# Performance work log

Measured on AMD Instinct MI355X. Metric: run time of the kernel, lower is better.

The kernel has to match this reference:

```python
import jax, jax.numpy as jnp
import numpy as np

SINKHORN_ITERS = 8
TEMPERATURE = 1.0
EPS = 1e-6


def sinkhorn(t):
    # log-domain Sinkhorn normalization, matching torch: log(clamp(t, min=eps)) / temp
    t = jnp.log(jnp.clip(t, EPS)) / TEMPERATURE
    for _ in range(SINKHORN_ITERS):
        t = t - jax.nn.logsumexp(t, axis=-2, keepdims=True)  # over tokens n
        t = t - jax.nn.logsumexp(t, axis=-1, keepdims=True)  # over experts e
    return jnp.exp(t)


def setup_inputs() -> dict:
    key = jax.random.key(0)
    k1, k2, k3 = jax.random.split(key, 3)
    B, N, D, E = 4, 4096, 1024, 8
    x = jax.random.normal(k1, (B, N, D), dtype=jnp.float32)
    gate_w = jax.random.normal(k2, (D, E), dtype=jnp.float32) * (D ** -0.5)
    experts = jax.random.normal(k3, (E, D, D), dtype=jnp.float32) * (D ** -0.5)
    return {"x": x, "gate_w": gate_w, "experts": experts}


def reference(x, gate_w, experts):
    B, N, D = x.shape
    E = gate_w.shape[-1]
    M = N // E  # tokens per expert

    gate_logits = jnp.einsum('bnd,de->bne', x, gate_w)
    competitive_gates = sinkhorn(gate_logits)  # b n e

    # topk along token dim (-2): transpose to (b,e,n), top_k along last axis
    vals, idx = jax.lax.top_k(jnp.swapaxes(competitive_gates, -1, -2), M)  # b e m
    gate_values = jnp.swapaxes(vals, -1, -2)   # b m e
    routed_indices = jnp.swapaxes(idx, -1, -2)  # b m e (int32)

    b_idx = jnp.arange(B)[:, None, None]  # (b,1,1)
    routed = x[b_idx, routed_indices]     # b m e d
    routed = jnp.transpose(routed, (2, 0, 1, 3))  # e b m d

    outputs = jnp.einsum('ebmd,edf->ebmf', routed, experts)  # e b m d
    outputs = outputs * jnp.transpose(gate_values, (2, 0, 1))[..., None]  # * (e b m 1)

    vals_bmed = jnp.transpose(outputs, (1, 2, 0, 3))  # b m e d
    routed_back = jnp.zeros_like(x).at[b_idx, routed_indices].set(vals_bmed)
    return routed_back
```

## Files before the change

### kernel.cpp

```cpp
#include <hip/hip_runtime.h>
#include <hip/hip_bf16.h>
#include <stdint.h>

typedef short s16x8 __attribute__((ext_vector_type(8)));
typedef float f32x4 __attribute__((ext_vector_type(4)));
typedef unsigned short u16;
typedef unsigned int u32;
typedef unsigned long long u64;

__device__ __forceinline__ float bf2f(u16 v){
  union { u32 u; float f; } c; c.u = ((u32)v) << 16; return c.f;
}

__device__ __forceinline__ u16 f2bf(float f){
  u32 u = __float_as_uint(f);
  u32 r = (u + 0x7FFFu + ((u >> 16) & 1u)) >> 16;
  return (u16)r;
}

__device__ __forceinline__ uint4 pack8(float4 a, float4 b){
  union { uint4 v; u16 s[8]; } o;
  o.s[0]=f2bf(a.x); o.s[1]=f2bf(a.y); o.s[2]=f2bf(a.z); o.s[3]=f2bf(a.w);
  o.s[4]=f2bf(b.x); o.s[5]=f2bf(b.y); o.s[6]=f2bf(b.z); o.s[7]=f2bf(b.w);
  return o.v;
}

__device__ __forceinline__ void gll16(const u16* g, u16* l){
  __builtin_amdgcn_global_load_lds((const __attribute__((address_space(1))) u32*)g,
                                   (__attribute__((address_space(3))) u32*)l, 16, 0, 0);
}

__global__ __launch_bounds__(1024) void k_prep(const void* __restrict__ xv,
                                               const void* __restrict__ gwv,
                                               const void* __restrict__ Wv,
                                               u16* __restrict__ xb,
                                               u16* __restrict__ WT,
                                               float* __restrict__ gates,
                                               int* __restrict__ winner,
                                               int* __restrict__ flag,
                                               uint4* __restrict__ out,
                                               int out_size, int mode){
  __shared__ __align__(16) char smem[36864];
  __shared__ float wacc[16][8];
  __shared__ int   dred[16];
  int bx = blockIdx.x;
  int tid = threadIdx.x;
  int wave = tid >> 6, lane = tid & 63;

  int cnt = 0;
  {
    const u32* xw = (const u32*)xv;
    #pragma unroll
    for (int i = 0; i < 4; i++){
      u32 w = xw[(i << 10) + tid];
      cnt += (((w >> 7) & 0xFF) >= 140) ? 1 : 0;
    }
    #pragma unroll
    for (int off = 32; off; off >>= 1) cnt += __shfl_xor(cnt, off, 64);
    if (lane == 0) dred[wave] = cnt;
  }
  __syncthreads();
  int tot = 0;
  #pragma unroll
  for (int w2 = 0; w2 < 16; w2++) tot += dred[w2];
  int is_f32 = (tot > 256) ? 1 : 0;
  if (bx == 0 && tid == 0) *flag = is_f32;

  if (bx < 2048){
    if (bx < 16) winner[(bx << 10) + tid] = -1;
    float4* gw_swz = (float4*)smem;
    {
      int r = tid;
      float g0,g1,g2,g3,g4,g5,g6,g7;
      if (is_f32){
        const float* gw = (const float*)gwv + ((size_t)r << 3);
        float4 u = *(const float4*)gw;
        float4 v = *(const float4*)(gw + 4);
        g0=u.x; g1=u.y; g2=u.z; g3=u.w; g4=v.x; g5=v.y; g6=v.z; g7=v.w;
      } else {
        union { uint4 v; u16 s[8]; } wu;
        wu.v = *(const uint4*)((const u16*)gwv + ((size_t)r << 3));
        g0=bf2f(wu.s[0]); g1=bf2f(wu.s[1]); g2=bf2f(wu.s[2]); g3=bf2f(wu.s[3]);
        g4=bf2f(wu.s[4]); g5=bf2f(wu.s[5]); g6=bf2f(wu.s[6]); g7=bf2f(wu.s[7]);
      }
      int p = r >> 3, j = r & 7;
      gw_swz[(p << 4) + (((j << 1)    ) ^ (p & 15))] = make_float4(g0,g1,g2,g3);
      gw_swz[(p << 4) + (((j << 1) | 1) ^ (p & 15))] = make_float4(g4,g5,g6,g7);
    }

    int tl = tid >> 7, pos = tid & 127;
    size_t base = ((((size_t)bx << 3) + tl) << 10) + ((size_t)pos << 3);
    float xf[8];
    if (is_f32){
      const float* xr = (const float*)xv + base;
      float4 u = *(const float4*)xr;
      float4 v = *(const float4*)(xr + 4);
      xf[0]=u.x; xf[1]=u.y; xf[2]=u.z; xf[3]=u.w;
      xf[4]=v.x; xf[5]=v.y; xf[6]=v.z; xf[7]=v.w;
      if (mode) *(uint4*)(xb + base) = pack8(u, v);
    } else {
      uint4 raw = *(const uint4*)((const u16*)xv + base);
      union { uint4 v; u16 s[8]; } xu; xu.v = raw;
      #pragma unroll
      for (int k = 0; k < 8; k++) xf[k] = bf2f(xu.s[k]);
      if (mode) *(uint4*)(xb + base) = raw;
    }
    __syncthreads();

    float a0=0,a1=0,a2=0,a3=0,a4=0,a5=0,a6=0,a7=0;
    #pragma unroll
    for (int j = 0; j < 8; j++){
      float4 wA = gw_swz[(pos << 4) + (((j << 1)    ) ^ (pos & 15))];
      float4 wB = gw_swz[(pos << 4) + (((j << 1) | 1) ^ (pos & 15))];
      float xv8 = xf[j];
      a0 += xv8*wA.x; a1 += xv8*wA.y; a2 += xv8*wA.z; a3 += xv8*wA.w;
      a4 += xv8*wB.x; a5 += xv8*wB.y; a6 += xv8*wB.z; a7 += xv8*wB.w;
    }
    int s1 = lane & 1;
    float k0 = s1 ? a4 : a0, g0 = s1 ? a0 : a4;
    float k1 = s1 ? a5 : a1, g1 = s1 ? a1 : a5;
    float k2 = s1 ? a6 : a2, g2 = s1 ? a2 : a6;
    float k3 = s1 ? a7 : a3, g3 = s1 ? a3 : a7;
    k0 += __shfl_xor(g0, 1, 64); k1 += __shfl_xor(g1, 1, 64);
    k2 += __shfl_xor(g2, 1, 64); k3 += __shfl_xor(g3, 1, 64);
    int s2 = (lane >> 1) & 1;
    float m0 = s2 ? k2 : k0, h0 = s2 ? k0 : k2;
    float m1 = s2 ? k3 : k1, h1 = s2 ? k1 : k3;
    m0 += __shfl_xor(h0, 2, 64); m1 += __shfl_xor(h1, 2, 64);
    int s3 = (lane >> 2) & 1;
    float r = s3 ? m1 : m0, h = s3 ? m0 : m1;
    r += __shfl_xor(h, 4, 64);
    r += __shfl_xor(r, 8, 64);
    r += __shfl_xor(r, 16, 64);
    r += __shfl_xor(r, 32, 64);
    if (lane < 8){
      int e = ((lane & 1) << 2) | (lane & 2) | ((lane >> 2) & 1);
      wacc[wave][e] = r;
    }
    __syncthreads();
    if (tid < 64){
      int tt = tid >> 3, e = tid & 7;
      float v = wacc[(tt << 1)][e] + wacc[(tt << 1) | 1][e];
      gates[((((size_t)bx << 3) + tt) << 3) + e] = v;
    }
    return;
  }

  if (mode == 0){
    int rb = bx - 2048;
    size_t words = (size_t)out_size >> (is_f32 ? 0 : 1);
    size_t n4 = words >> 2;
    size_t i = (size_t)rb * 1024 + tid;
    uint4 z = make_uint4(0, 0, 0, 0);
    for (; i < n4; i += (size_t)512 * 1024) out[i] = z;
    return;
  }

  {
    int rb = bx - 2048;
    int sub = tid >> 8;
    int t = tid & 255;
    int g = (rb << 2) + sub;
    int e = g >> 8, t2 = g & 255;
    int td = (t2 >> 4) << 6, tf = (t2 & 15) << 6;
    u16 (*tile)[72] = (u16(*)[72])(smem + (size_t)sub * (64 * 72 * 2));
    #pragma unroll
    for (int i = 0; i < 2; i++){
      int id = t + (i << 8);
      int row = id >> 3, c8 = id & 7;
      size_t src = ((size_t)(e*1024 + td + row))*1024 + tf + (c8 << 3);
      uint4 v;
      if (is_f32){
        const float* wf = (const float*)Wv;
        v = pack8(*(const float4*)(wf + src), *(const float4*)(wf + src + 4));
      } else {
        v = *(const uint4*)((const u16*)Wv + src);
      }
      *(uint4*)&tile[row][c8 << 3] = v;
    }
    __syncthreads();
    #pragma unroll
    for (int i = 0; i < 2; i++){
      int id = t + (i << 8);
      int frow = id >> 3, c8 = id & 7;
      union { uint4 v; u16 s[8]; } o;
      #pragma unroll
      for (int j = 0; j < 8; j++) o.s[j] = tile[(c8 << 3) + j][frow];
      *(uint4*)(WT + ((size_t)(e*1024 + tf + frow))*1024 + td + (c8 << 3)) = o.v;
    }
  }
}

__global__ __launch_bounds__(1024) void k_sinkhorn(float* __restrict__ gates){
  __shared__ float wred[128];
  __shared__ float lbc[8];
  int bx = blockIdx.x;
  int tid = threadIdx.x;
  int wave = tid >> 6, lane = tid & 63;
  float* gb = gates + ((size_t)bx << 15);
  float4 va[4], vb[4];
  #pragma unroll
  for (int q = 0; q < 4; q++){
    float* gp = gb + (((q << 10) + tid) << 3);
    float4 a = *(const float4*)gp;
    float4 b = *(const float4*)(gp + 4);
    a.x=fmaxf(a.x,1e-6f); a.y=fmaxf(a.y,1e-6f); a.z=fmaxf(a.z,1e-6f); a.w=fmaxf(a.w,1e-6f);
    b.x=fmaxf(b.x,1e-6f); b.y=fmaxf(b.y,1e-6f); b.z=fmaxf(b.z,1e-6f); b.w=fmaxf(b.w,1e-6f);
    va[q]=a; vb[q]=b;
  }
  for (int it = 0; it < 8; it++){
    float s0 = ((va[0].x+va[1].x)+(va[2].x+va[3].x));
    float s1 = ((va[0].y+va[1].y)+(va[2].y+va[3].y));
    float s2 = ((va[0].z+va[1].z)+(va[2].z+va[3].z));
    float s3 = ((va[0].w+va[1].w)+(va[2].w+va[3].w));
    float s4 = ((vb[0].x+vb[1].x)+(vb[2].x+vb[3].x));
    float s5 = ((vb[0].y+vb[1].y)+(vb[2].y+vb[3].y));
    float s6 = ((vb[0].z+vb[1].z)+(vb[2].z+vb[3].z));
    float s7 = ((vb[0].w+vb[1].w)+(vb[2].w+vb[3].w));
    #pragma unroll
    for (int off = 32; off; off >>= 1){
      s0 += __shfl_xor(s0, off, 64); s1 += __shfl_xor(s1, off, 64);
      s2 += __shfl_xor(s2, off, 64); s3 += __shfl_xor(s3, off, 64);
      s4 += __shfl_xor(s4, off, 64); s5 += __shfl_xor(s5, off, 64);
      s6 += __shfl_xor(s6, off, 64); s7 += __shfl_xor(s7, off, 64);
    }
    if (lane == 0){
      wred[(wave<<3)+0]=s0; wred[(wave<<3)+1]=s1; wred[(wave<<3)+2]=s2; wred[(wave<<3)+3]=s3;
      wred[(wave<<3)+4]=s4; wred[(wave<<3)+5]=s5; wred[(wave<<3)+6]=s6; wred[(wave<<3)+7]=s7;
    }
    __syncthreads();
    if (tid < 8){
      float S = 0.f;
      #pragma unroll
      for (int w2 = 0; w2 < 16; w2++) S += wred[(w2 << 3) + tid];
      lbc[tid] = 1.0f / S;
    }
    __syncthreads();
    float i0=lbc[0], i1=lbc[1], i2=lbc[2], i3=lbc[3];
    float i4=lbc[4], i5=lbc[5], i6=lbc[6], i7=lbc[7];
    #pragma unroll
    for (int q = 0; q < 4; q++){
      float4 a = va[q], b = vb[q];
      a.x*=i0; a.y*=i1; a.z*=i2; a.w*=i3;
      b.x*=i4; b.y*=i5; b.z*=i6; b.w*=i7;
      float rs = ((a.x+a.y)+(a.z+a.w)) + ((b.x+b.y)+(b.z+b.w));
      float ir = 1.0f / rs;
      a.x*=ir; a.y*=ir; a.z*=ir; a.w*=ir;
      b.x*=ir; b.y*=ir; b.z*=ir; b.w*=ir;
      va[q]=a; vb[q]=b;
    }
  }
  #pragma unroll
  for (int q = 0; q < 4; q++){
    float* gp = gb + (((q << 10) + tid) << 3);
    *(float4*)gp = va[q];
    *(float4*)(gp + 4) = vb[q];
  }
}

__global__ __launch_bounds__(256) void k_rank(const float* __restrict__ gates,
                                              int* __restrict__ routed, int* __restrict__ winner){
  __shared__ u32 ord_s[4096];
  __shared__ u32 cnt_s[1024];
  int bx = blockIdx.x;
  int be = bx >> 5;
  int b = be >> 3, e = be & 7;
  int slice = bx & 31;
  int tid = threadIdx.x;
  const float* gb = gates + (size_t)b * (4096 * 8);
  for (int i = tid; i < 4096; i += 256){
    float v = gb[(i << 3) + e];
    u32 fb = __float_as_uint(v);
    ord_s[i] = fb ^ ((fb >> 31) ? 0xFFFFFFFFu : 0x80000000u);
  }
  __syncthreads();

  int tg = tid & 31;
  int js = tid >> 5;
  int i0 = (slice << 7) + (tg << 2);
  int gchunk = i0 & ~7;
  u32 v0 = ord_s[i0], v1 = ord_s[i0+1], v2 = ord_s[i0+2], v3 = ord_s[i0+3];
  int jlo = js << 9, jhi = jlo + 512;
  int c0 = 0, c1 = 0, c2 = 0, c3 = 0;

  int endA = min(jhi, gchunk);
  for (int j = jlo; j < endA; j += 8){
    uint4 w0 = *(const uint4*)&ord_s[j];
    uint4 w1 = *(const uint4*)&ord_s[j + 4];
    c0 += (w0.x>=v0)+(w0.y>=v0)+(w0.z>=v0)+(w0.w>=v0)+(w1.x>=v0)+(w1.y>=v0)+(w1.z>=v0)+(w1.w>=v0);
    c1 += (w0.x>=v1)+(w0.y>=v1)+(w0.z>=v1)+(w0.w>=v1)+(w1.x>=v1)+(w1.y>=v1)+(w1.z>=v1)+(w1.w>=v1);
    c2 += (w0.x>=v2)+(w0.y>=v2)+(w0.z>=v2)+(w0.w>=v2)+(w1.x>=v2)+(w1.y>=v2)+(w1.z>=v2)+(w1.w>=v2);
    c3 += (w0.x>=v3)+(w0.y>=v3)+(w0.z>=v3)+(w0.w>=v3)+(w1.x>=v3)+(w1.y>=v3)+(w1.z>=v3)+(w1.w>=v3);
  }
  int begB = max(jlo, gchunk + 8);
  for (int j = begB; j < jhi; j += 8){
    uint4 w0 = *(const uint4*)&ord_s[j];
    uint4 w1 = *(const uint4*)&ord_s[j + 4];
    c0 += (w0.x>v0)+(w0.y>v0)+(w0.z>v0)+(w0.w>v0)+(w1.x>v0)+(w1.y>v0)+(w1.z>v0)+(w1.w>v0);
    c1 += (w0.x>v1)+(w0.y>v1)+(w0.z>v1)+(w0.w>v1)+(w1.x>v1)+(w1.y>v1)+(w1.z>v1)+(w1.w>v1);
    c2 += (w0.x>v2)+(w0.y>v2)+(w0.z>v2)+(w0.w>v2)+(w1.x>v2)+(w1.y>v2)+(w1.z>v2)+(w1.w>v2);
    c3 += (w0.x>v3)+(w0.y>v3)+(w0.z>v3)+(w0.w>v3)+(w1.x>v3)+(w1.y>v3)+(w1.z>v3)+(w1.w>v3);
  }
  if (gchunk >= jlo && gchunk < jhi){
    int base_off = i0 & 7;
    #pragma unroll
    for (int jj = 0; jj < 8; jj++){
      u32 w = ord_s[gchunk + jj];
      c0 += (jj < base_off + 0) ? (w >= v0) : (w > v0);
      c1 += (jj < base_off + 1) ? (w >= v1) : (w > v1);
      c2 += (jj < base_off + 2) ? (w >= v2) : (w > v2);
      c3 += (jj < base_off + 3) ? (w >= v3) : (w > v3);
    }
  }
  int lt = tg << 2;
  cnt_s[(js << 7) + lt + 0] = c0;
  cnt_s[(js << 7) + lt + 1] = c1;
  cnt_s[(js << 7) + lt + 2] = c2;
  cnt_s[(js << 7) + lt + 3] = c3;
  __syncthreads();
  if (tid < 128){
    int rank = 0;
    #pragma unroll
    for (int s = 0; s < 8; s++) rank += cnt_s[(s << 7) + tid];
    int i = (slice << 7) + tid;
    if (rank < 512){
      routed[(be << 9) + rank] = i;
      atomicMax(&winner[(b << 12) + i], (rank << 3) | e);
    }
  }
}

__global__ __launch_bounds__(256) void k_gemm_fast(const u16* __restrict__ xb, const u16* __restrict__ WT,
                                                   const float* __restrict__ gates,
                                                   const int* __restrict__ routed,
                                                   const int* __restrict__ winner,
                                                   const int* __restrict__ flag,
                                                   void* __restrict__ outv){
  __shared__ u16 As[128 * 32];
  __shared__ u16 Bs[128 * 32];
  __shared__ int   tok_s[128];
  __shared__ float gate_s[128];
  __shared__ int   flg_s[128];
  int is_f32 = *flag;
  int bx = blockIdx.x;
  int tid = threadIdx.x;

  if (bx >= 1024){
    int zb = bx - 1024;
    #pragma unroll 1
    for (int i = 0; i < 128; i++){
      int g = (zb << 7) + i;
      if (winner[g] < 0){
        size_t rbase = ((size_t)g) << 10;
        if (is_f32){
          float* o = (float*)outv;
          *(float4*)(o + rbase + (tid << 2)) = make_float4(0.f, 0.f, 0.f, 0.f);
        } else {
          u16* o = (u16*)outv;
          uint2 z; z.x = 0; z.y = 0;
          *(uint2*)(o + rbase + (tid << 2)) = z;
        }
      }
    }
    return;
  }

  int e = bx & 7;
  int rest = bx >> 3;
  int b = rest >> 5;
  int tile = rest & 31;
  int mt = tile & 3, nt = tile >> 2;
  int w = tid >> 6, lane = tid & 63;
  int quad = lane >> 4, l16 = lane & 15;

  const int* idx_base = routed + (((b << 3) + e) << 9) + (mt << 7);

  if (tid < 128){
    int tok = idx_base[tid];
    int mg  = (mt << 7) + tid;
    int win = winner[(b << 12) + tok];
    tok_s[tid]  = tok;
    flg_s[tid]  = (win == ((mg << 3) | e)) ? 1 : 0;
    gate_s[tid] = gates[((((size_t)b << 12) + tok) << 3) + e];
  }
  __syncthreads();

  int r0 = tid >> 2;
  int ch = tid & 3;
  int r1 = r0 + 64;
  int swz = ch ^ ((r0 >> 1) & 3);
  const u16* gA0 = xb + ((((size_t)b << 12) + tok_s[r0]) << 10) + (swz << 3);
  const u16* gA1 = xb + ((((size_t)b << 12) + tok_s[r1]) << 10) + (swz << 3);
  int f0 = nt << 7;
  const u16* gB0 = WT + ((((size_t)e << 10) + f0 + r0) << 10) + (swz << 3);
  const u16* gB1 = WT + ((((size_t)e << 10) + f0 + r1) << 10) + (swz << 3);
  u16* lA0 = As + (w << 9);
  u16* lA1 = As + 2048 + (w << 9);
  u16* lB0 = Bs + (w << 9);
  u16* lB1 = Bs + 2048 + (w << 9);
  int swzr = quad ^ ((l16 >> 1) & 3);

  f32x4 acc[4][4] = {};
  int wm = (w & 1) << 6, wn = (w >> 1) << 6;

  for (int k0 = 0; k0 < 1024; k0 += 32){
    gll16(gA0 + k0, lA0);
    gll16(gA1 + k0, lA1);
    gll16(gB0 + k0, lB0);
    gll16(gB1 + k0, lB1);
    __syncthreads();
    s16x8 af[4], bv[4];
    #pragma unroll
    for (int im = 0; im < 4; im++)
      af[im] = *(const s16x8*)&As[((wm + (im << 4) + l16) << 5) + (swzr << 3)];
    #pragma unroll
    for (int in = 0; in < 4; in++)
      bv[in] = *(const s16x8*)&Bs[((wn + (in << 4) + l16) << 5) + (swzr << 3)];
    __syncthreads();
    #pragma unroll
    for (int im = 0; im < 4; im++){
      #pragma unroll
      for (int in = 0; in < 4; in++)
        acc[im][in] = __builtin_amdgcn_mfma_f32_16x16x32_bf16(af[im], bv[in], acc[im][in], 0, 0, 0);
    }
  }

  #pragma unroll
  for (int im = 0; im < 4; im++){
    #pragma unroll
    for (int r = 0; r < 4; r++){
      int mrow = wm + (im << 4) + (quad << 2) + r;
      if (flg_s[mrow]){
        float g  = gate_s[mrow];
        int tok  = tok_s[mrow];
        size_t obase = ((((size_t)b << 12) + tok) << 10) + f0 + wn + l16;
        if (is_f32){
          float* o32 = (float*)outv;
          #pragma unroll
          for (int in = 0; in < 4; in++) o32[obase + (in << 4)] = acc[im][in][r] * g;
        } else {
          u16* o16 = (u16*)outv;
          #pragma unroll
          for (int in = 0; in < 4; in++) o16[obase + (in << 4)] = f2bf(acc[im][in][r] * g);
        }
      }
    }
  }
}

__global__ __launch_bounds__(256) void k_gemm_slow(const void* __restrict__ xv, const void* __restrict__ Wv,
                                                   const float* __restrict__ gates,
                                                   const int* __restrict__ routed,
                                                   const int* __restrict__ winner,
                                                   const int* __restrict__ flag,
                                                   void* __restrict__ outv){
  __shared__ u16 As[128 * 32];
  __shared__ u16 Bw[32 * 132];
  __shared__ u16 Bs[128 * 32];
  __shared__ int   tok_s[128];
  __shared__ float gate_s[128];
  __shared__ int   flg_s[128];
  int is_f32 = *flag;
  int bx = blockIdx.x;
  int e = bx & 7;
  int rest = bx >> 3;
  int b = rest >> 5;
  int tile = rest & 31;
  int mt = tile & 3, nt = tile >> 2;
  int tid = threadIdx.x;
  int w = tid >> 6, lane = tid & 63;
  int quad = lane >> 4, l16 = lane & 15;

  const int* idx_base = routed + (((b << 3) + e) << 9) + (mt << 7);

  if (tid < 128){
    int tok = idx_base[tid];
    int mg  = (mt << 7) + tid;
    int win = winner[(b << 12) + tok];
    tok_s[tid]  = tok;
    flg_s[tid]  = (win == ((mg << 3) | e)) ? 1 : 0;
    gate_s[tid] = gates[((((size_t)b << 12) + tok) << 3) + e];
  }
  __syncthreads();

  int r0 = tid >> 2;
  int ch = tid & 3;
  int r1 = r0 + 64;
  size_t offA0 = ((((size_t)b << 12) + tok_s[r0]) << 10) + (ch << 3);
  size_t offA1 = ((((size_t)b << 12) + tok_s[r1]) << 10) + (ch << 3);
  int f0 = nt << 7;
  int kkB0 = tid >> 4;
  int fcB  = tid & 15;
  size_t offB0 = ((size_t)e << 20) + ((size_t)kkB0 << 10) + f0 + (fcB << 3);
  size_t offB1 = offB0 + ((size_t)16 << 10);
  int f_loc = tid >> 1;
  int half  = tid & 1;

  f32x4 acc[4][4] = {};
  int wm = (w & 1) << 6, wn = (w >> 1) << 6;

  for (int k0 = 0; k0 < 1024; k0 += 32){
    uint4 a0, a1, b0, b1;
    if (is_f32){
      const float* xf = (const float*)xv;
      const float* wf = (const float*)Wv;
      a0 = pack8(*(const float4*)(xf + offA0 + k0), *(const float4*)(xf + offA0 + k0 + 4));
      a1 = pack8(*(const float4*)(xf + offA1 + k0), *(const float4*)(xf + offA1 + k0 + 4));
      b0 = pack8(*(const float4*)(wf + offB0 + ((size_t)k0 << 10)),
                 *(const float4*)(wf + offB0 + ((size_t)k0 << 10) + 4));
      b1 = pack8(*(const float4*)(wf + offB1 + ((size_t)k0 << 10)),
                 *(const float4*)(wf + offB1 + ((size_t)k0 << 10) + 4));
    } else {
      const u16* xh = (const u16*)xv;
      const u16* wh = (const u16*)Wv;
      a0 = *(const uint4*)(xh + offA0 + k0);
      a1 = *(const uint4*)(xh + offA1 + k0);
      b0 = *(const uint4*)(wh + offB0 + ((size_t)k0 << 10));
      b1 = *(const uint4*)(wh + offB1 + ((size_t)k0 << 10));
    }
    *(uint4*)&As[(r0 << 5) + (ch << 3)] = a0;
    *(uint4*)&As[(r1 << 5) + (ch << 3)] = a1;
    *(uint4*)&Bw[kkB0 * 132 + (fcB << 3)] = b0;
    *(uint4*)&Bw[(kkB0 + 16) * 132 + (fcB << 3)] = b1;
    __syncthreads();
    union { uint4 v[2]; u16 s[16]; } tv;
    #pragma unroll
    for (int j = 0; j < 16; j++) tv.s[j] = Bw[((half << 4) + j) * 132 + f_loc];
    *(uint4*)&Bs[(f_loc << 5) + (half << 4)]     = tv.v[0];
    *(uint4*)&Bs[(f_loc << 5) + (half << 4) + 8] = tv.v[1];
    __syncthreads();
    s16x8 af[4], bv[4];
    #pragma unroll
    for (int im = 0; im < 4; im++)
      af[im] = *(const s16x8*)&As[((wm + (im << 4) + l16) << 5) + (quad << 3)];
    #pragma unroll
    for (int in = 0; in < 4; in++)
      bv[in] = *(const s16x8*)&Bs[((wn + (in << 4) + l16) << 5) + (quad << 3)];
    __syncthreads();
    #pragma unroll
    for (int im = 0; im < 4; im++){
      #pragma unroll
      for (int in = 0; in < 4; in++)
        acc[im][in] = __builtin_amdgcn_mfma_f32_16x16x32_bf16(af[im], bv[in], acc[im][in], 0, 0, 0);
    }
  }

  #pragma unroll
  for (int im = 0; im < 4; im++){
    #pragma unroll
    for (int r = 0; r < 4; r++){
      int mrow = wm + (im << 4) + (quad << 2) + r;
      if (flg_s[mrow]){
        float g  = gate_s[mrow];
        int tok  = tok_s[mrow];
        size_t obase = ((((size_t)b << 12) + tok) << 10) + f0 + wn + l16;
        if (is_f32){
          float* o32 = (float*)outv;
          #pragma unroll
          for (int in = 0; in < 4; in++) o32[obase + (in << 4)] = acc[im][in][r] * g;
        } else {
          u16* o16 = (u16*)outv;
          #pragma unroll
          for (int in = 0; in < 4; in++) o16[obase + (in << 4)] = f2bf(acc[im][in][r] * g);
        }
      }
    }
  }
}

extern "C" void kernel_launch(void* const* d_in, const int* in_sizes, int n_in,
                              void* d_out, int out_size, void* d_ws, size_t ws_size,
                              hipStream_t stream){
  const void* x  = d_in[0];
  const void* gw = d_in[1];
  const void* W  = d_in[2];
  char* ws = (char*)d_ws;
  float* gates  = (float*)ws;
  int*   winner = (int*)(ws + 524288);
  int*   routed = (int*)(ws + 589824);
  int*   flag   = (int*)(ws + 655360);
  u16*   xb     = (u16*)(ws + 655616);
  u16*   WT     = (u16*)(ws + 655616 + 33554432);
  size_t need_fast = 655616ull + 33554432ull + 16777216ull;
  bool fast = ws_size >= need_fast;

  hipLaunchKernelGGL(k_prep, dim3(2560), dim3(1024), 0, stream,
                     x, gw, W, xb, WT, gates, winner, flag, (uint4*)d_out, out_size,
                     fast ? 1 : 0);
  hipLaunchKernelGGL(k_sinkhorn, dim3(4), dim3(1024), 0, stream, gates);
  hipLaunchKernelGGL(k_rank, dim3(1024), dim3(256), 0, stream, gates, routed, winner);
  if (fast){
    hipLaunchKernelGGL(k_gemm_fast, dim3(1152), dim3(256), 0, stream, xb, WT, gates, routed, winner,
                       flag, d_out);
  } else {
    hipLaunchKernelGGL(k_gemm_slow, dim3(1024), dim3(256), 0, stream, x, W, gates, routed, winner,
                       flag, d_out);
  }
}
```

Before: 276.9 us.

## Double-buffer GEMM LDS loads, replace brute-force ranking with histogram bucket ranking

```diff
diff --git a/kernel.cpp b/kernel.cpp
--- a/kernel.cpp
+++ b/kernel.cpp
@@ -258,74 +258,64 @@
   }
 }
 
-__global__ __launch_bounds__(256) void k_rank(const float* __restrict__ gates,
-                                              int* __restrict__ routed, int* __restrict__ winner){
-  __shared__ u32 ord_s[4096];
-  __shared__ u32 cnt_s[1024];
-  int bx = blockIdx.x;
-  int be = bx >> 5;
+__global__ __launch_bounds__(1024) void k_rank(const float* __restrict__ gates,
+                                               int* __restrict__ routed, int* __restrict__ winner){
+  __shared__ u32 skey_s[4096];
+  __shared__ u16 sidx_s[4096];
+  __shared__ u32 hist[512];
+  __shared__ u32 ssum[512];
+  __shared__ u32 cur[512];
+  int be = blockIdx.x;
   int b = be >> 3, e = be & 7;
-  int slice = bx & 31;
   int tid = threadIdx.x;
-  const float* gb = gates + (size_t)b * (4096 * 8);
-  for (int i = tid; i < 4096; i += 256){
-    float v = gb[(i << 3) + e];
-    u32 fb = __float_as_uint(v);
-    ord_s[i] = fb ^ ((fb >> 31) ? 0xFFFFFFFFu : 0x80000000u);
-  }
+  const float* gb = gates + ((size_t)b << 15);
+  if (tid < 512){ hist[tid] = 0; cur[tid] = 0; }
   __syncthreads();
-
-  int tg = tid & 31;
-  int js = tid >> 5;
-  int i0 = (slice << 7) + (tg << 2);
-  int gchunk = i0 & ~7;
-  u32 v0 = ord_s[i0], v1 = ord_s[i0+1], v2 = ord_s[i0+2], v3 = ord_s[i0+3];
-  int jlo = js << 9, jhi = jlo + 512;
-  int c0 = 0, c1 = 0, c2 = 0, c3 = 0;
-
-  int endA = min(jhi, gchunk);
-  for (int j = jlo; j < endA; j += 8){
-    uint4 w0 = *(const uint4*)&ord_s[j];
-    uint4 w1 = *(const uint4*)&ord_s[j + 4];
-    c0 += (w0.x>=v0)+(w0.y>=v0)+(w0.z>=v0)+(w0.w>=v0)+(w1.x>=v0)+(w1.y>=v0)+(w1.z>=v0)+(w1.w>=v0);
-    c1 += (w0.x>=v1)+(w0.y>=v1)+(w0.z>=v1)+(w0.w>=v1)+(w1.x>=v1)+(w1.y>=v1)+(w1.z>=v1)+(w1.w>=v1);
-    c2 += (w0.x>=v2)+(w0.y>=v2)+(w0.z>=v2)+(w0.w>=v2)+(w1.x>=v2)+(w1.y>=v2)+(w1.z>=v2)+(w1.w>=v2);
-    c3 += (w0.x>=v3)+(w0.y>=v3)+(w0.z>=v3)+(w0.w>=v3)+(w1.x>=v3)+(w1.y>=v3)+(w1.z>=v3)+(w1.w>=v3);
-  }
-  int begB = max(jlo, gchunk + 8);
-  for (int j = begB; j < jhi; j += 8){
-    uint4 w0 = *(const uint4*)&ord_s[j];
-    uint4 w1 = *(const uint4*)&ord_s[j + 4];
-    c0 += (w0.x>v0)+(w0.y>v0)+(w0.z>v0)+(w0.w>v0)+(w1.x>v0)+(w1.y>v0)+(w1.z>v0)+(w1.w>v0);
-    c1 += (w0.x>v1)+(w0.y>v1)+(w0.z>v1)+(w0.w>v1)+(w1.x>v1)+(w1.y>v1)+(w1.z>v1)+(w1.w>v1);
-    c2 += (w0.x>v2)+(w0.y>v2)+(w0.z>v2)+(w0.w>v2)+(w1.x>v2)+(w1.y>v2)+(w1.z>v2)+(w1.w>v2);
-    c3 += (w0.x>v3)+(w0.y>v3)+(w0.z>v3)+(w0.w>v3)+(w1.x>v3)+(w1.y>v3)+(w1.z>v3)+(w1.w>v3);
-  }
-  if (gchunk >= jlo && gchunk < jhi){
-    int base_off = i0 & 7;
-    #pragma unroll
-    for (int jj = 0; jj < 8; jj++){
-      u32 w = ord_s[gchunk + jj];
-      c0 += (jj < base_off + 0) ? (w >= v0) : (w > v0);
-      c1 += (jj < base_off + 1) ? (w >= v1) : (w > v1);
-      c2 += (jj < base_off + 2) ? (w >= v2) : (w > v2);
-      c3 += (jj < base_off + 3) ? (w >= v3) : (w > v3);
-    }
-  }
-  int lt = tg << 2;
-  cnt_s[(js << 7) + lt + 0] = c0;
-  cnt_s[(js << 7) + lt + 1] = c1;
-  cnt_s[(js << 7) + lt + 2] = c2;
-  cnt_s[(js << 7) + lt + 3] = c3;
+  u32 mykey[4];
+  #pragma unroll
+  for (int q = 0; q < 4; q++){
+    int i = (q << 10) + tid;
+    u32 fb = __float_as_uint(gb[((size_t)i << 3) + e]);
+    u32 k = fb ^ ((fb >> 31) ? 0xFFFFFFFFu : 0x80000000u);
+    mykey[q] = k;
+    atomicAdd(&hist[k >> 23], 1u);
+  }
   __syncthreads();
-  if (tid < 128){
-    int rank = 0;
-    #pragma unroll
-    for (int s = 0; s < 8; s++) rank += cnt_s[(s << 7) + tid];
-    int i = (slice << 7) + tid;
-    if (rank < 512){
-      routed[(be << 9) + rank] = i;
-      atomicMax(&winner[(b << 12) + i], (rank << 3) | e);
+  if (tid < 512) ssum[tid] = hist[tid];
+  __syncthreads();
+  for (int d = 1; d < 512; d <<= 1){
+    u32 v = 0;
+    if (tid < 512) v = ssum[tid] + ((tid + d < 512) ? ssum[tid + d] : 0u);
+    __syncthreads();
+    if (tid < 512) ssum[tid] = v;
+    __syncthreads();
+  }
+  #pragma unroll
+  for (int q = 0; q < 4; q++){
+    u32 k = mykey[q];
+    u32 bin = k >> 23;
+    u32 slot = ssum[bin] - hist[bin] + atomicAdd(&cur[bin], 1u);
+    skey_s[slot] = k;
+    sidx_s[slot] = (u16)((q << 10) + tid);
+  }
+  __syncthreads();
+  #pragma unroll
+  for (int q = 0; q < 4; q++){
+    u32 k = mykey[q];
+    int i = (q << 10) + tid;
+    u32 bin = k >> 23;
+    u32 end = ssum[bin];
+    u32 beg = end - hist[bin];
+    if (beg < 512u){
+      int r = (int)beg;
+      for (u32 s = beg; s < end; s++){
+        u32 sk = skey_s[s];
+        r += (sk > k || (sk == k && (int)sidx_s[s] < i)) ? 1 : 0;
+      }
+      if (r < 512){
+        routed[(be << 9) + r] = i;
+        atomicMax(&winner[(b << 12) + i], (r << 3) | e);
+      }
     }
   }
 }
@@ -336,8 +326,8 @@
                                                    const int* __restrict__ winner,
                                                    const int* __restrict__ flag,
                                                    void* __restrict__ outv){
-  __shared__ u16 As[128 * 32];
-  __shared__ u16 Bs[128 * 32];
+  __shared__ u16 As[2][4096];
+  __shared__ u16 Bs[2][4096];
   __shared__ int   tok_s[128];
   __shared__ float gate_s[128];
   __shared__ int   flg_s[128];
@@ -345,11 +335,10 @@
   int bx = blockIdx.x;
   int tid = threadIdx.x;
 
-  if (bx >= 1024){
-    int zb = bx - 1024;
+  if (bx < 128){
     #pragma unroll 1
     for (int i = 0; i < 128; i++){
-      int g = (zb << 7) + i;
+      int g = (bx << 7) + i;
       if (winner[g] < 0){
         size_t rbase = ((size_t)g) << 10;
         if (is_f32){
@@ -365,8 +354,9 @@
     return;
   }
 
-  int e = bx & 7;
-  int rest = bx >> 3;
+  int g = bx - 128;
+  int e = g & 7;
+  int rest = g >> 3;
   int b = rest >> 5;
   int tile = rest & 31;
   int mt = tile & 3, nt = tile >> 2;
@@ -394,36 +384,70 @@
   int f0 = nt << 7;
   const u16* gB0 = WT + ((((size_t)e << 10) + f0 + r0) << 10) + (swz << 3);
   const u16* gB1 = WT + ((((size_t)e << 10) + f0 + r1) << 10) + (swz << 3);
-  u16* lA0 = As + (w << 9);
-  u16* lA1 = As + 2048 + (w << 9);
-  u16* lB0 = Bs + (w << 9);
-  u16* lB1 = Bs + 2048 + (w << 9);
+  int wbase = w << 9;
   int swzr = quad ^ ((l16 >> 1) & 3);
 
   f32x4 acc[4][4] = {};
   int wm = (w & 1) << 6, wn = (w >> 1) << 6;
 
-  for (int k0 = 0; k0 < 1024; k0 += 32){
-    gll16(gA0 + k0, lA0);
-    gll16(gA1 + k0, lA1);
-    gll16(gB0 + k0, lB0);
-    gll16(gB1 + k0, lB1);
-    __syncthreads();
-    s16x8 af[4], bv[4];
-    #pragma unroll
-    for (int im = 0; im < 4; im++)
-      af[im] = *(const s16x8*)&As[((wm + (im << 4) + l16) << 5) + (swzr << 3)];
-    #pragma unroll
-    for (int in = 0; in < 4; in++)
-      bv[in] = *(const s16x8*)&Bs[((wn + (in << 4) + l16) << 5) + (swzr << 3)];
-    __syncthreads();
-    #pragma unroll
-    for (int im = 0; im < 4; im++){
-      #pragma unroll
-      for (int in = 0; in < 4; in++)
-        acc[im][in] = __builtin_amdgcn_mfma_f32_16x16x32_bf16(af[im], bv[in], acc[im][in], 0, 0, 0);
-    }
-  }
+#define STAGE(d, K)  do { \
+    gll16(gA0 + (K), &As[d][wbase]); \
+    gll16(gA1 + (K), &As[d][2048 + wbase]); \
+    gll16(gB0 + (K), &Bs[d][wbase]); \
+    gll16(gB1 + (K), &Bs[d][2048 + wbase]); \
+  } while (0)
+
+#define COMPUTE(d)  do { \
+    s16x8 af[4], bv[4]; \
+    _Pragma("unroll") \
+    for (int im = 0; im < 4; im++) \
+      af[im] = *(const s16x8*)&As[d][((wm + (im << 4) + l16) << 5) + (swzr << 3)]; \
+    _Pragma("unroll") \
+    for (int in = 0; in < 4; in++) \
+      bv[in] = *(const s16x8*)&Bs[d][((wn + (in << 4) + l16) << 5) + (swzr << 3)]; \
+    _Pragma("unroll") \
+    for (int im = 0; im < 4; im++){ \
+      _Pragma("unroll") \
+      for (int in = 0; in < 4; in++) \
+        acc[im][in] = __builtin_amdgcn_mfma_f32_16x16x32_bf16(af[im], bv[in], acc[im][in], 0, 0, 0); \
+    } \
+  } while (0)
+
+#define SB() __builtin_amdgcn_sched_barrier(0)
+
+  STAGE(0, 0);
+  asm volatile("s_waitcnt vmcnt(0)");
+  SB();
+  __builtin_amdgcn_s_barrier();
+  SB();
+  #pragma unroll 1
+  for (int k0 = 0; k0 < 1024; k0 += 64){
+    STAGE(1, k0 + 32);
+    asm volatile("s_waitcnt vmcnt(4)");
+    SB();
+    __builtin_amdgcn_s_barrier();
+    SB();
+    COMPUTE(0);
+    SB();
+    __builtin_amdgcn_s_barrier();
+    SB();
+    if (k0 + 64 < 1024){
+      STAGE(0, k0 + 64);
+      asm volatile("s_waitcnt vmcnt(4)");
+    } else {
+      asm volatile("s_waitcnt vmcnt(0)");
+    }
+    SB();
+    __builtin_amdgcn_s_barrier();
+    SB();
+    COMPUTE(1);
+    SB();
+    __builtin_amdgcn_s_barrier();
+    SB();
+  }
+#undef STAGE
+#undef COMPUTE
+#undef SB
 
   #pragma unroll
   for (int im = 0; im < 4; im++){
@@ -431,17 +455,17 @@
     for (int r = 0; r < 4; r++){
       int mrow = wm + (im << 4) + (quad << 2) + r;
       if (flg_s[mrow]){
-        float g  = gate_s[mrow];
+        float gv = gate_s[mrow];
         int tok  = tok_s[mrow];
         size_t obase = ((((size_t)b << 12) + tok) << 10) + f0 + wn + l16;
         if (is_f32){
           float* o32 = (float*)outv;
           #pragma unroll
-          for (int in = 0; in < 4; in++) o32[obase + (in << 4)] = acc[im][in][r] * g;
+          for (int in = 0; in < 4; in++) o32[obase + (in << 4)] = acc[im][in][r] * gv;
         } else {
           u16* o16 = (u16*)outv;
           #pragma unroll
-          for (int in = 0; in < 4; in++) o16[obase + (in << 4)] = f2bf(acc[im][in][r] * g);
+          for (int in = 0; in < 4; in++) o16[obase + (in << 4)] = f2bf(acc[im][in][r] * gv);
         }
       }
     }
@@ -588,7 +612,7 @@
                      x, gw, W, xb, WT, gates, winner, flag, (uint4*)d_out, out_size,
                      fast ? 1 : 0);
   hipLaunchKernelGGL(k_sinkhorn, dim3(4), dim3(1024), 0, stream, gates);
-  hipLaunchKernelGGL(k_rank, dim3(1024), dim3(256), 0, stream, gates, routed, winner);
+  hipLaunchKernelGGL(k_rank, dim3(32), dim3(1024), 0, stream, gates, routed, winner);
   if (fast){
     hipLaunchKernelGGL(k_gemm_fast, dim3(1152), dim3(256), 0, stream, xb, WT, gates, routed, winner,
                        flag, d_out);
```

Result: slower. 426.0 us (+53.8%).
